# Kernel tuning notes

Measured on AMD Instinct MI355X. Metric: run time of the kernel, lower is better.

## Reference

```python
import jax, jax.numpy as jnp
import numpy as np

B, Q = 4, 65536
LATENT = 256
FEAT = 32
RES = 64
HID = [256, 256, 256]
TRIDIM = 3 * FEAT * RES * RES  # 393216


def _bilinear_sample(plane, xy):
    """F.grid_sample equivalent: bilinear, padding_mode='border', align_corners=True.
    plane: [C, H, W]; xy: [Q, 2] with xy[:,0]=x (width), xy[:,1]=y (height), in [-1,1].
    Returns [Q, C]."""
    C, H, W = plane.shape
    x = (xy[:, 0] + 1.0) * 0.5 * (W - 1)  # align_corners=True mapping
    y = (xy[:, 1] + 1.0) * 0.5 * (H - 1)
    x0 = jnp.floor(x)
    y0 = jnp.floor(y)
    wx = x - x0
    wy = y - y0
    x0i = jnp.clip(x0.astype(jnp.int32), 0, W - 1)
    x1i = jnp.clip(x0i + 1, 0, W - 1)  # border padding via clamp
    y0i = jnp.clip(y0.astype(jnp.int32), 0, H - 1)
    y1i = jnp.clip(y0i + 1, 0, H - 1)
    v00 = plane[:, y0i, x0i]  # [C, Q]
    v01 = plane[:, y0i, x1i]
    v10 = plane[:, y1i, x0i]
    v11 = plane[:, y1i, x1i]
    top = v00 * (1.0 - wx) + v01 * wx
    bot = v10 * (1.0 - wx) + v11 * wx
    return (top * (1.0 - wy) + bot * wy).T  # [Q, C]


def _sample_triplanes(triplanes, pts):
    """triplanes: [3, C, R, R]; pts: [Q, 3] clamped to [-1,1]. Returns [Q, 3C]."""
    xy = _bilinear_sample(triplanes[0], pts[:, jnp.array([0, 1])])
    xz = _bilinear_sample(triplanes[1], pts[:, jnp.array([0, 2])])
    yz = _bilinear_sample(triplanes[2], pts[:, jnp.array([1, 2])])
    return jnp.concatenate([xy, xz, yz], axis=-1)


def setup_inputs() -> dict:
    key = jax.random.key(0)
    ks = jax.random.split(key, 20)
    d_in_mlp = 3 * FEAT + 3  # 99

    def lin(k, i, o):
        k1, k2 = jax.random.split(k)
        s = 1.0 / np.sqrt(i)
        return (jax.random.uniform(k1, (i, o), jnp.float32, -s, s),
                jax.random.uniform(k2, (o,), jnp.float32, -s, s))

    w1, b1 = lin(ks[0], LATENT, 2 * LATENT)
    w2, b2 = lin(ks[1], 2 * LATENT, TRIDIM)
    mw0, mb0 = lin(ks[2], d_in_mlp, HID[0])
    mw1, mb1 = lin(ks[3], HID[0], HID[1])
    mw2, mb2 = lin(ks[4], HID[1], HID[2])
    sdf_w, sdf_b = lin(ks[5], HID[2], 1)
    occ_w, occ_b = lin(ks[6], HID[2], 1)

    z_sample = jax.random.normal(ks[7], (B, LATENT), jnp.float32)
    query_points = jax.random.uniform(ks[8], (B, Q, 3), jnp.float32) * 2.0 - 1.0

    return {"z_sample": z_sample, "query_points": query_points,
            "w1": w1, "b1": b1, "w2": w2, "b2": b2,
            "mw0": mw0, "mb0": mb0, "mw1": mw1, "mb1": mb1,
            "mw2": mw2, "mb2": mb2,
            "sdf_w": sdf_w, "sdf_b": sdf_b, "occ_w": occ_w, "occ_b": occ_b}


def reference(z_sample, query_points, w1, b1, w2, b2, mw0, mb0, mw1, mb1,
              mw2, mb2, sdf_w, sdf_b, occ_w, occ_b):
    # triplane head: Linear -> SiLU -> Linear, reshaped to [B, 3, C, R, R]
    h = jax.nn.silu(z_sample @ w1 + b1)
    triplanes = (h @ w2 + b2).reshape(B, 3, FEAT, RES, RES)

    pts = jnp.clip(query_points, -1.0, 1.0)  # clamp only for sampling
    query_feats = jax.vmap(_sample_triplanes)(triplanes, pts)  # [B, Q, 3C]

    x = jnp.concatenate([query_feats, query_points], axis=-1)  # [B, Q, 3C+3]
    x = jax.nn.silu(x @ mw0 + mb0)
    x = jax.nn.silu(x @ mw1 + mb1)
    x = jax.nn.silu(x @ mw2 + mb2)
    sdf_pred = x @ sdf_w + sdf_b
    occ_logits = x @ occ_w + occ_b
    return triplanes, sdf_pred, occ_logits
```

## Files before the change

### kernel.cpp

```cpp
#include <hip/hip_runtime.h>
#include <cstdint>

#define BQ 4
#define QPB 65536
#define QTOT (BQ*QPB)
#define TRIN 393216
#define TRI_OUT (BQ*TRIN)

#define X0LD 272
#define ACTLD 528

typedef __attribute__((ext_vector_type(8))) __bf16 bf16x8;
typedef __attribute__((ext_vector_type(4))) float f32x4;
typedef __attribute__((ext_vector_type(2))) float f32x2;

__device__ __forceinline__ unsigned short f2bf(float f) {
    unsigned u = __float_as_uint(f);
    u += 0x7fffu + ((u >> 16) & 1u);
    return (unsigned short)(u >> 16);
}
__device__ __forceinline__ float bflo(unsigned u) {
    return __uint_as_float(u << 16);
}
__device__ __forceinline__ float bfhi(unsigned u) {
    return __uint_as_float(u & 0xffff0000u);
}
__device__ __forceinline__ f32x2 lohi2(unsigned u) {
    f32x2 r; r[0] = bflo(u); r[1] = bfhi(u); return r;
}
__device__ __forceinline__ f32x2 mk2(float a, float b) {
    f32x2 r; r[0] = a; r[1] = b; return r;
}
__device__ __forceinline__ f32x2 fma2(f32x2 a, f32x2 b, f32x2 c) {
    return __builtin_elementwise_fma(a, b, c);
}
__device__ __forceinline__ unsigned cvt_pk_bf16(float lo, float hi) {
    unsigned r;
    asm("v_cvt_pk_bf16_f32 %0, %1, %2" : "=v"(r) : "v"(lo), "v"(hi));
    return r;
}
__device__ __forceinline__ float fast_rcp(float d) {
    float r;
    asm("v_rcp_f32 %0, %1" : "=v"(r) : "v"(d));
    return r;
}
__device__ __forceinline__ float silu_f(float x) {
    return x * fast_rcp(1.0f + __expf(-x));
}
__device__ __forceinline__ f32x2 silu2(f32x2 x) {
    f32x2 e; e[0] = __expf(-x[0]); e[1] = __expf(-x[1]);
    f32x2 one = {1.f, 1.f};
    f32x2 d = e + one;
    f32x2 r; r[0] = fast_rcp(d[0]); r[1] = fast_rcp(d[1]);
    return x * r;
}
__device__ __forceinline__ int c_true(int p) {
    return (p & ~63) + ((p & 3) * 16 + ((p & 63) >> 2));
}

__global__ __launch_bounds__(256) void k_prep(
    const float* __restrict__ mw0, const float* __restrict__ mw1, const float* __restrict__ mw2,
    const float* __restrict__ sdf_w, const float* __restrict__ occ_w,
    const float* __restrict__ z, const float* __restrict__ w1, const float* __restrict__ b1,
    unsigned short* __restrict__ wt0, unsigned short* __restrict__ wt1,
    unsigned short* __restrict__ wt2, float* __restrict__ sdfp, float* __restrict__ occp,
    float* __restrict__ hout)
{
    int idx = blockIdx.x * 256 + threadIdx.x;
    if (idx < 163840) {
        const float* src;
        unsigned short* dst;
        int rel;
        bool perm;
        int kmax;
        if (idx < 32768)       { rel = idx;         src = mw0; dst = wt0; perm = false; kmax = 99;  }
        else if (idx < 98304)  { rel = idx - 32768; src = mw1; dst = wt1; perm = true;  kmax = 256; }
        else                   { rel = idx - 98304; src = mw2; dst = wt2; perm = true;  kmax = 256; }
        int e  = rel & 7;
        int kg = (rel >> 3) & 3;
        int n  = (rel >> 5) & 255;
        int t  = rel >> 13;
        int ks = t * 32 + kg * 8 + e;
        int k  = perm ? c_true(ks) : ks;
        float v = (ks < kmax) ? src[k * 256 + n] : 0.0f;
        dst[rel] = f2bf(v);
    } else if (idx < 164352) {
        int r = idx - 163840;
        int p = r & 255, which = r >> 8;
        float v = (which ? occ_w : sdf_w)[c_true(p)];
        (which ? occp : sdfp)[p] = v;
    } else if (idx < 166400) {
        int gid = idx - 164352;
        int b = gid >> 9, n = gid & 511;
        float acc = b1[n];
        #pragma unroll 8
        for (int k = 0; k < 256; ++k)
            acc += z[b * 256 + k] * w1[k * 512 + n];
        hout[gid] = silu_f(acc);
    }
}

__global__ __launch_bounds__(256) void k_triplane(
    const float* __restrict__ w2, const float* __restrict__ b2,
    const float* __restrict__ h, float* __restrict__ outTri,
    unsigned short* __restrict__ triT)
{
    __shared__ float hs[2048];
    int t = threadIdx.x;
    ((float4*)hs)[t]       = ((const float4*)h)[t];
    ((float4*)hs)[t + 256] = ((const float4*)h)[t + 256];
    __syncthreads();
    int g = blockIdx.x * 256 + t;
    int j = g * 2;
    const float* wj = w2 + j;
    float ax[4] = {0.f, 0.f, 0.f, 0.f}, ay[4] = {0.f, 0.f, 0.f, 0.f};

    for (int k0 = 0; k0 < 512; k0 += 8) {
        float2 wv[8];
        #pragma unroll
        for (int u = 0; u < 8; ++u)
            wv[u] = *(const float2*)(wj + (size_t)(k0 + u) * TRIN);
        float4 hv[4][2];
        #pragma unroll
        for (int b = 0; b < 4; ++b) {
            hv[b][0] = *(const float4*)&hs[b * 512 + k0];
            hv[b][1] = *(const float4*)&hs[b * 512 + k0 + 4];
        }
        #pragma unroll
        for (int b = 0; b < 4; ++b) {
            ax[b] += hv[b][0].x * wv[0].x + hv[b][0].y * wv[1].x
                   + hv[b][0].z * wv[2].x + hv[b][0].w * wv[3].x
                   + hv[b][1].x * wv[4].x + hv[b][1].y * wv[5].x
                   + hv[b][1].z * wv[6].x + hv[b][1].w * wv[7].x;
            ay[b] += hv[b][0].x * wv[0].y + hv[b][0].y * wv[1].y
                   + hv[b][0].z * wv[2].y + hv[b][0].w * wv[3].y
                   + hv[b][1].x * wv[4].y + hv[b][1].y * wv[5].y
                   + hv[b][1].z * wv[6].y + hv[b][1].w * wv[7].y;
        }
    }

    float2 bj = *(const float2*)(b2 + j);
    int x = j & 63, y = (j >> 6) & 63, c = (j >> 12) & 31, p = j >> 17;
    int ttb = ((p * 64 + y) * 64 + x) * 32 + c;
    #pragma unroll
    for (int b = 0; b < 4; ++b) {
        float vX = ax[b] + bj.x, vY = ay[b] + bj.y;
        float2 o; o.x = vX; o.y = vY;
        *(float2*)(outTri + (size_t)b * TRIN + j) = o;
        unsigned short* tb = triT + b * TRIN + ttb;
        tb[0]  = f2bf(vX);
        tb[32] = f2bf(vY);
    }
}

template<int K, bool INPLACE, int LDIN>
__device__ __forceinline__ void mlp_layer(
    const unsigned char* bin, unsigned char* bout,
    const unsigned short* __restrict__ wtp, const float* __restrict__ mb,
    int lane, int c4)
{
    const int l15 = lane & 15;
    const int kg = lane >> 4;
    const int n0 = c4 * 64;
    const unsigned char* abase = bin + l15 * LDIN + kg * 16;
    const unsigned short* wbase = wtp + (((n0 + l15) * 4 + kg) << 3);
    f32x4 acc[4][4];
    #pragma unroll
    for (int rf = 0; rf < 4; ++rf)
        #pragma unroll
        for (int cf = 0; cf < 4; ++cf) {
            f32x4 zv = {0.f, 0.f, 0.f, 0.f};
            acc[rf][cf] = zv;
        }
    uint4 av[4], bv[4];
    #pragma unroll
    for (int rf = 0; rf < 4; ++rf)
        av[rf] = *(const uint4*)(abase + rf * 16 * LDIN);
    #pragma unroll
    for (int cf = 0; cf < 4; ++cf)
        bv[cf] = *(const uint4*)(wbase + (cf * 16 * 4 << 3));
    #pragma unroll
    for (int t = 0; t < K / 32; ++t) {
        uint4 avn[4], bvn[4];
        if (t + 1 < K / 32) {
            #pragma unroll
            for (int rf = 0; rf < 4; ++rf)
                avn[rf] = *(const uint4*)(abase + rf * 16 * LDIN + (t + 1) * 64);
            #pragma unroll
            for (int cf = 0; cf < 4; ++cf)
                bvn[cf] = *(const uint4*)(wbase + ((((t + 1) * 256 + cf * 16) * 4) << 3));
        }
        __builtin_amdgcn_s_setprio(1);
        #pragma unroll
        for (int rf = 0; rf < 4; ++rf)
            #pragma unroll
            for (int cf = 0; cf < 4; ++cf)
                acc[rf][cf] = __builtin_amdgcn_mfma_f32_16x16x32_bf16(
                    __builtin_bit_cast(bf16x8, av[rf]),
                    __builtin_bit_cast(bf16x8, bv[cf]),
                    acc[rf][cf], 0, 0, 0);
        __builtin_amdgcn_s_setprio(0);
        if (t + 1 < K / 32) {
            #pragma unroll
            for (int i = 0; i < 4; ++i) { av[i] = avn[i]; bv[i] = bvn[i]; }
        }
    }
    if (INPLACE) __syncthreads();
    float bias[4];
    #pragma unroll
    for (int cf = 0; cf < 4; ++cf) bias[cf] = mb[n0 + 16 * cf + l15];
    unsigned char* sbase = bout + kg * 4 * ACTLD + (n0 + l15 * 4) * 2;
    #pragma unroll
    for (int rf = 0; rf < 4; ++rf) {
        f32x2 bA = mk2(bias[0], bias[0]), bB = mk2(bias[1], bias[1]);
        f32x2 bC = mk2(bias[2], bias[2]), bD = mk2(bias[3], bias[3]);
        f32x2 sA0 = silu2(__builtin_shufflevector(acc[rf][0], acc[rf][0], 0, 1) + bA);
        f32x2 sA1 = silu2(__builtin_shufflevector(acc[rf][0], acc[rf][0], 2, 3) + bA);
        f32x2 sB0 = silu2(__builtin_shufflevector(acc[rf][1], acc[rf][1], 0, 1) + bB);
        f32x2 sB1 = silu2(__builtin_shufflevector(acc[rf][1], acc[rf][1], 2, 3) + bB);
        f32x2 sC0 = silu2(__builtin_shufflevector(acc[rf][2], acc[rf][2], 0, 1) + bC);
        f32x2 sC1 = silu2(__builtin_shufflevector(acc[rf][2], acc[rf][2], 2, 3) + bC);
        f32x2 sD0 = silu2(__builtin_shufflevector(acc[rf][3], acc[rf][3], 0, 1) + bD);
        f32x2 sD1 = silu2(__builtin_shufflevector(acc[rf][3], acc[rf][3], 2, 3) + bD);
        uint2 pk;
        pk.x = cvt_pk_bf16(sA0[0], sB0[0]); pk.y = cvt_pk_bf16(sC0[0], sD0[0]);
        *(uint2*)(sbase + (rf * 16 + 0) * ACTLD) = pk;
        pk.x = cvt_pk_bf16(sA0[1], sB0[1]); pk.y = cvt_pk_bf16(sC0[1], sD0[1]);
        *(uint2*)(sbase + (rf * 16 + 1) * ACTLD) = pk;
        pk.x = cvt_pk_bf16(sA1[0], sB1[0]); pk.y = cvt_pk_bf16(sC1[0], sD1[0]);
        *(uint2*)(sbase + (rf * 16 + 2) * ACTLD) = pk;
        pk.x = cvt_pk_bf16(sA1[1], sB1[1]); pk.y = cvt_pk_bf16(sC1[1], sD1[1]);
        *(uint2*)(sbase + (rf * 16 + 3) * ACTLD) = pk;
    }
    __syncthreads();
}

__global__ __launch_bounds__(256) void k_mlp(
    const float* __restrict__ qp, const unsigned short* __restrict__ triT,
    const unsigned short* __restrict__ wt0, const unsigned short* __restrict__ wt1,
    const unsigned short* __restrict__ wt2,
    const float* __restrict__ mb0, const float* __restrict__ mb1, const float* __restrict__ mb2,
    const float* __restrict__ sdfp, const float* __restrict__ sdf_b,
    const float* __restrict__ occp, const float* __restrict__ occ_b,
    float* __restrict__ out)
{
    __shared__ __align__(16) unsigned char lds[64 * X0LD + 64 * ACTLD];
    unsigned char* x0  = lds;
    unsigned char* act = lds + 64 * X0LD;
    unsigned char* scr = act;
    const int t = threadIdx.x;

    const int bid = blockIdx.x;
    const int xcd = bid & 7;
    const int batch = xcd >> 1;
    const int brow = (bid >> 3) + ((xcd & 1) << 9);
    const int row0 = batch * QPB + brow * 64;

    if (t < 192) {
        int plane = t >> 6, q = t & 63;
        int gr = row0 + q;
        float px = qp[3 * gr], py = qp[3 * gr + 1], pz = qp[3 * gr + 2];
        float u = (plane == 2) ? py : px;
        float v = (plane == 0) ? py : pz;
        u = fminf(fmaxf(u, -1.f), 1.f);
        v = fminf(fmaxf(v, -1.f), 1.f);
        float xf = (u + 1.f) * 31.5f;
        float yf = (v + 1.f) * 31.5f;
        float x0f = floorf(xf), y0f = floorf(yf);
        float wx = xf - x0f, wy = yf - y0f;
        int xi = min(max((int)x0f, 0), 63);
        int yi = min(max((int)y0f, 0), 63);
        int xi1 = min(xi + 1, 63), yi1 = min(yi + 1, 63);
        int pb = (batch * 3 + plane) * 64;
        int4 offs;
        offs.x = ((pb + yi ) * 64 + xi ) << 6;
        offs.y = ((pb + yi ) * 64 + xi1) << 6;
        offs.z = ((pb + yi1) * 64 + xi ) << 6;
        offs.w = ((pb + yi1) * 64 + xi1) << 6;
        float4 w;
        w.x = (1.f - wx) * (1.f - wy); w.y = wx * (1.f - wy);
        w.z = (1.f - wx) * wy;         w.w = wx * wy;
        *(int4*)(scr + t * 32) = offs;
        *(float4*)(scr + t * 32 + 16) = w;
        if (plane == 0) {
            uint4 c0;
            c0.x = (unsigned)f2bf(px) | ((unsigned)f2bf(py) << 16);
            c0.y = (unsigned)f2bf(pz);
            c0.z = 0u; c0.w = 0u;
            uint4 z4; z4.x = z4.y = z4.z = z4.w = 0u;
            *(uint4*)(x0 + q * X0LD + 192) = c0;
            *(uint4*)(x0 + q * X0LD + 208) = z4;
            *(uint4*)(x0 + q * X0LD + 224) = z4;
            *(uint4*)(x0 + q * X0LD + 240) = z4;
        }
    }
    __syncthreads();

    const char* tb8 = (const char*)triT;
    #pragma unroll
    for (int i = 0; i < 3; ++i) {
        int unit = i * 256 + t;
        int chunk = unit & 3;
        int uc = unit >> 2;
        const unsigned char* ce = scr + uc * 32;
        int4 offs = *(const int4*)ce;
        float4 w = *(const float4*)(ce + 16);
        int cb = chunk * 16;
        uint4 c0 = *(const uint4*)(tb8 + offs.x + cb);
        uint4 c1 = *(const uint4*)(tb8 + offs.y + cb);
        uint4 c2 = *(const uint4*)(tb8 + offs.z + cb);
        uint4 c3 = *(const uint4*)(tb8 + offs.w + cb);
        const unsigned* u0 = (const unsigned*)&c0;
        const unsigned* u1 = (const unsigned*)&c1;
        const unsigned* u2 = (const unsigned*)&c2;
        const unsigned* u3 = (const unsigned*)&c3;
        f32x2 wx2 = mk2(w.x, w.x), wy2 = mk2(w.y, w.y);
        f32x2 wz2 = mk2(w.z, w.z), ww2 = mk2(w.w, w.w);
        unsigned r[4];
        #pragma unroll
        for (int q2 = 0; q2 < 4; ++q2) {
            f32x2 s = wx2 * lohi2(u0[q2]);
            s = fma2(wy2, lohi2(u1[q2]), s);
            s = fma2(wz2, lohi2(u2[q2]), s);
            s = fma2(ww2, lohi2(u3[q2]), s);
            r[q2] = cvt_pk_bf16(s[0], s[1]);
        }
        int q = uc & 63, plane = uc >> 6;
        uint4 pk; pk.x = r[0]; pk.y = r[1]; pk.z = r[2]; pk.w = r[3];
        *(uint4*)(x0 + q * X0LD + plane * 64 + chunk * 16) = pk;
    }
    __syncthreads();

    const int lane = t & 63;
    const int c4 = t >> 6;

    mlp_layer<128, false, X0LD >(x0,  act, wt0, mb0, lane, c4);
    mlp_layer<256, true,  ACTLD>(act, act, wt1, mb1, lane, c4);
    mlp_layer<256, true,  ACTLD>(act, act, wt2, mb2, lane, c4);

    {
        const int l15 = lane & 15;
        const int kg = lane >> 4;
        int row = c4 * 16 + l15;
        int gr = row0 + row;
        const unsigned char* hbase = act + row * ACTLD + kg * 128;
        f32x2 aS2 = mk2(0.f, 0.f), aO2 = mk2(0.f, 0.f);
        int kb = kg * 64;
        #pragma unroll
        for (int i = 0; i < 8; ++i) {
            int k = kb + i * 8;
            uint4 xv = *(const uint4*)(hbase + i * 16);
            const unsigned* xu = (const unsigned*)&xv;
            float4 s0 = *(const float4*)(sdfp + k);
            float4 s1 = *(const float4*)(sdfp + k + 4);
            float4 o0 = *(const float4*)(occp + k);
            float4 o1 = *(const float4*)(occp + k + 4);
            f32x2 xa = lohi2(xu[0]), xb = lohi2(xu[1]);
            f32x2 xc = lohi2(xu[2]), xd = lohi2(xu[3]);
            aS2 = fma2(xa, mk2(s0.x, s0.y), aS2);
            aS2 = fma2(xb, mk2(s0.z, s0.w), aS2);
            aS2 = fma2(xc, mk2(s1.x, s1.y), aS2);
            aS2 = fma2(xd, mk2(s1.z, s1.w), aS2);
            aO2 = fma2(xa, mk2(o0.x, o0.y), aO2);
            aO2 = fma2(xb, mk2(o0.z, o0.w), aO2);
            aO2 = fma2(xc, mk2(o1.x, o1.y), aO2);
            aO2 = fma2(xd, mk2(o1.z, o1.w), aO2);
        }
        float aS = aS2[0] + aS2[1];
        float aO = aO2[0] + aO2[1];
        aS += __shfl_xor(aS, 16);
        aS += __shfl_xor(aS, 32);
        aO += __shfl_xor(aO, 16);
        aO += __shfl_xor(aO, 32);
        if (kg == 0) {
            out[TRI_OUT + gr] = aS + sdf_b[0];
            out[TRI_OUT + QTOT + gr] = aO + occ_b[0];
        }
    }
}

extern "C" void kernel_launch(void* const* d_in, const int* in_sizes, int n_in,
                              void* d_out, int out_size, void* d_ws, size_t ws_size,
                              hipStream_t stream)
{
    const float* z     = (const float*)d_in[0];
    const float* qp    = (const float*)d_in[1];
    const float* w1    = (const float*)d_in[2];
    const float* b1    = (const float*)d_in[3];
    const float* w2    = (const float*)d_in[4];
    const float* b2    = (const float*)d_in[5];
    const float* mw0   = (const float*)d_in[6];
    const float* mb0   = (const float*)d_in[7];
    const float* mw1   = (const float*)d_in[8];
    const float* mb1   = (const float*)d_in[9];
    const float* mw2   = (const float*)d_in[10];
    const float* mb2   = (const float*)d_in[11];
    const float* sdf_w = (const float*)d_in[12];
    const float* sdf_b = (const float*)d_in[13];
    const float* occ_w = (const float*)d_in[14];
    const float* occ_b = (const float*)d_in[15];
    float* out = (float*)d_out;
    char* ws = (char*)d_ws;

    float* h_ws          = (float*)(ws);
    unsigned short* wt0  = (unsigned short*)(ws + 8192);
    unsigned short* wt1  = (unsigned short*)(ws + 73728);
    unsigned short* wt2  = (unsigned short*)(ws + 204800);
    float* sdfp          = (float*)(ws + 335872);
    float* occp          = (float*)(ws + 336896);
    unsigned short* triT = (unsigned short*)(ws + 337920);

    k_prep<<<650, 256, 0, stream>>>(mw0, mw1, mw2, sdf_w, occ_w, z, w1, b1,
                                    wt0, wt1, wt2, sdfp, occp, h_ws);
    k_triplane<<<768, 256, 0, stream>>>(w2, b2, h_ws, out, triT);
    k_mlp<<<4096, 256, 0, stream>>>(qp, triT, wt0, wt1, wt2,
                                    mb0, mb1, mb2, sdfp, sdf_b, occp, occ_b, out);
}
```

Measured before the change: 296.1 us.

## Merge input and activation LDS buffers and drop register prefetch in MLP layers

The separate x0 input tile is folded into the single activation buffer: the first layer now runs in place, and the sampling scratch moves into the unused tail columns of each activation row. This cuts LDS per block from about 51KB to about 33KB, so more blocks can fit per CU. The software double-buffering of A/B fragments inside the K loop is also removed, which lowers register pressure. The cost is an extra barrier before the first layer's writeback and less latency hiding in the MFMA loop.

```diff
diff --git a/kernel.cpp b/kernel.cpp
--- a/kernel.cpp
+++ b/kernel.cpp
@@ -7,7 +7,6 @@
 #define TRIN 393216
 #define TRI_OUT (BQ*TRIN)
 
-#define X0LD 272
 #define ACTLD 528
 
 typedef __attribute__((ext_vector_type(8))) __bf16 bf16x8;
@@ -153,17 +152,16 @@
     }
 }
 
-template<int K, bool INPLACE, int LDIN>
+template<int K, bool INPLACE>
 __device__ __forceinline__ void mlp_layer(
-    const unsigned char* bin, unsigned char* bout,
+    unsigned char* act,
     const unsigned short* __restrict__ wtp, const float* __restrict__ mb,
     int lane, int c4)
 {
     const int l15 = lane & 15;
     const int kg = lane >> 4;
     const int n0 = c4 * 64;
-    const unsigned char* abase = bin + l15 * LDIN + kg * 16;
-    const unsigned short* wbase = wtp + (((n0 + l15) * 4 + kg) << 3);
+    const unsigned char* abase = act + l15 * ACTLD + kg * 16;
     f32x4 acc[4][4];
     #pragma unroll
     for (int rf = 0; rf < 4; ++rf)
@@ -172,23 +170,16 @@
             f32x4 zv = {0.f, 0.f, 0.f, 0.f};
             acc[rf][cf] = zv;
         }
-    uint4 av[4], bv[4];
-    #pragma unroll
-    for (int rf = 0; rf < 4; ++rf)
-        av[rf] = *(const uint4*)(abase + rf * 16 * LDIN);
-    #pragma unroll
-    for (int cf = 0; cf < 4; ++cf)
-        bv[cf] = *(const uint4*)(wbase + (cf * 16 * 4 << 3));
     #pragma unroll
     for (int t = 0; t < K / 32; ++t) {
-        uint4 avn[4], bvn[4];
-        if (t + 1 < K / 32) {
-            #pragma unroll
-            for (int rf = 0; rf < 4; ++rf)
-                avn[rf] = *(const uint4*)(abase + rf * 16 * LDIN + (t + 1) * 64);
-            #pragma unroll
-            for (int cf = 0; cf < 4; ++cf)
-                bvn[cf] = *(const uint4*)(wbase + ((((t + 1) * 256 + cf * 16) * 4) << 3));
+        uint4 av[4], bv[4];
+        #pragma unroll
+        for (int rf = 0; rf < 4; ++rf)
+            av[rf] = *(const uint4*)(abase + rf * 16 * ACTLD + t * 64);
+        #pragma unroll
+        for (int cf = 0; cf < 4; ++cf) {
+            int n = n0 + 16 * cf + l15;
+            bv[cf] = *(const uint4*)(wtp + (((t * 256 + n) * 4 + kg) << 3));
         }
         __builtin_amdgcn_s_setprio(1);
         #pragma unroll
@@ -200,16 +191,12 @@
                     __builtin_bit_cast(bf16x8, bv[cf]),
                     acc[rf][cf], 0, 0, 0);
         __builtin_amdgcn_s_setprio(0);
-        if (t + 1 < K / 32) {
-            #pragma unroll
-            for (int i = 0; i < 4; ++i) { av[i] = avn[i]; bv[i] = bvn[i]; }
-        }
     }
     if (INPLACE) __syncthreads();
     float bias[4];
     #pragma unroll
     for (int cf = 0; cf < 4; ++cf) bias[cf] = mb[n0 + 16 * cf + l15];
-    unsigned char* sbase = bout + kg * 4 * ACTLD + (n0 + l15 * 4) * 2;
+    unsigned char* sbase = act + kg * 4 * ACTLD + (n0 + l15 * 4) * 2;
     #pragma unroll
     for (int rf = 0; rf < 4; ++rf) {
         f32x2 bA = mk2(bias[0], bias[0]), bB = mk2(bias[1], bias[1]);
@@ -244,10 +231,8 @@
     const float* __restrict__ occp, const float* __restrict__ occ_b,
     float* __restrict__ out)
 {
-    __shared__ __align__(16) unsigned char lds[64 * X0LD + 64 * ACTLD];
-    unsigned char* x0  = lds;
-    unsigned char* act = lds + 64 * X0LD;
-    unsigned char* scr = act;
+    __shared__ __align__(16) unsigned char act[64 * ACTLD];
+    #define SCR(u) (act + ((u) >> 3) * ACTLD + 256 + ((u) & 7) * 32)
     const int t = threadIdx.x;
 
     const int bid = blockIdx.x;
@@ -280,18 +265,18 @@
         float4 w;
         w.x = (1.f - wx) * (1.f - wy); w.y = wx * (1.f - wy);
         w.z = (1.f - wx) * wy;         w.w = wx * wy;
-        *(int4*)(scr + t * 32) = offs;
-        *(float4*)(scr + t * 32 + 16) = w;
+        *(int4*)SCR(t) = offs;
+        *(float4*)(SCR(t) + 16) = w;
         if (plane == 0) {
             uint4 c0;
             c0.x = (unsigned)f2bf(px) | ((unsigned)f2bf(py) << 16);
             c0.y = (unsigned)f2bf(pz);
             c0.z = 0u; c0.w = 0u;
             uint4 z4; z4.x = z4.y = z4.z = z4.w = 0u;
-            *(uint4*)(x0 + q * X0LD + 192) = c0;
-            *(uint4*)(x0 + q * X0LD + 208) = z4;
-            *(uint4*)(x0 + q * X0LD + 224) = z4;
-            *(uint4*)(x0 + q * X0LD + 240) = z4;
+            *(uint4*)(act + q * ACTLD + 192) = c0;
+            *(uint4*)(act + q * ACTLD + 208) = z4;
+            *(uint4*)(act + q * ACTLD + 224) = z4;
+            *(uint4*)(act + q * ACTLD + 240) = z4;
         }
     }
     __syncthreads();
@@ -302,7 +287,7 @@
         int unit = i * 256 + t;
         int chunk = unit & 3;
         int uc = unit >> 2;
-        const unsigned char* ce = scr + uc * 32;
+        const unsigned char* ce = SCR(uc);
         int4 offs = *(const int4*)ce;
         float4 w = *(const float4*)(ce + 16);
         int cb = chunk * 16;
@@ -327,16 +312,16 @@
         }
         int q = uc & 63, plane = uc >> 6;
         uint4 pk; pk.x = r[0]; pk.y = r[1]; pk.z = r[2]; pk.w = r[3];
-        *(uint4*)(x0 + q * X0LD + plane * 64 + chunk * 16) = pk;
+        *(uint4*)(act + q * ACTLD + plane * 64 + chunk * 16) = pk;
     }
     __syncthreads();
 
     const int lane = t & 63;
     const int c4 = t >> 6;
 
-    mlp_layer<128, false, X0LD >(x0,  act, wt0, mb0, lane, c4);
-    mlp_layer<256, true,  ACTLD>(act, act, wt1, mb1, lane, c4);
-    mlp_layer<256, true,  ACTLD>(act, act, wt2, mb2, lane, c4);
+    mlp_layer<128, true>(act, wt0, mb0, lane, c4);
+    mlp_layer<256, true>(act, wt1, mb1, lane, c4);
+    mlp_layer<256, true>(act, wt2, mb2, lane, c4);
 
     {
         const int l15 = lane & 15;
@@ -377,6 +362,7 @@
             out[TRI_OUT + QTOT + gr] = aO + occ_b[0];
         }
     }
+    #undef SCR
 }
 
 extern "C" void kernel_launch(void* const* d_in, const int* in_sizes, int n_in,
```

After: 304.1 us. 2.7% more time.
